# Kernel tuning notes

Hardware: AMD Instinct MI355X
Metric: run time of the kernel (lower is better)

## Reference

```python
import jax, jax.numpy as jnp
import numpy as np
import math

IN_CH = 256
OUT_CH = 256
N_JOINTS = 25
BATCH = 16384


def setup_inputs() -> dict:
    key = jax.random.key(0)
    kx, kw = jax.random.split(key)
    x = jax.random.normal(kx, (N_JOINTS, BATCH, IN_CH), dtype=jnp.float32)
    stdv = 1.0 / math.sqrt(OUT_CH)
    weight = jax.random.uniform(kw, (IN_CH, OUT_CH), dtype=jnp.float32,
                                minval=-stdv, maxval=stdv)
    return {"x": x, "weight": weight}


def reference(x, weight):
    # x: (N, B, D) -> attention over joints N per batch element
    xb = jnp.transpose(x, (1, 0, 2))            # (B, N, D)
    s3 = jnp.einsum('bnd,bmd->bnm', xb, xb)     # (B, N, N) self-similarity
    s = jax.nn.softmax(s3, axis=-1)
    out = jnp.einsum('bnm,bmd->bnd', s, xb)     # (B, N, D)
    out = out @ weight                           # (B, N, out_channels)
    return out
```

## Files before the change

kernel.cpp:

```cpp
#include <hip/hip_runtime.h>

#define GRID   1024
#define BLOCK  256
#define BATCH  16384
#define NJ     25
#define DEPTH  256
#define ITERS  (BATCH / GRID)

typedef short s16x8 __attribute__((ext_vector_type(8)));
typedef short s16x4 __attribute__((ext_vector_type(4)));
typedef float f32x4 __attribute__((ext_vector_type(4)));

__device__ __forceinline__ short f2bf(float f) {
  union { float f; unsigned u; } c; c.f = f;
  unsigned r = (c.u + 0x7FFFu + ((c.u >> 16) & 1u)) >> 16;
  return (short)r;
}

#define MFMA(a, b, c) __builtin_amdgcn_mfma_f32_16x16x32_bf16((a), (b), (c), 0, 0, 0)

__global__ __launch_bounds__(BLOCK, 2)
void geo_gcn_fused(const float* __restrict__ x,
                   const float* __restrict__ w,
                   float* __restrict__ out)
{
  __shared__ short As[32][256];
  __shared__ short Ps[32][40];
  __shared__ float S3[32][36];
  __shared__ short Yt[4][64][32];

  const int tid  = threadIdx.x;
  const int wv   = tid >> 6;
  const int lane = tid & 63;
  const int quad = lane >> 4;
  const int l16  = lane & 15;

  s16x8 wf[8][4];
  {
    const int ncol = wv * 64 + l16;
#pragma unroll
    for (int ks = 0; ks < 8; ++ks)
#pragma unroll
      for (int td = 0; td < 4; ++td) {
        const float* wp = w + (size_t)(ks * 32 + quad * 8) * DEPTH + ncol + td * 16;
#pragma unroll
        for (int j = 0; j < 8; ++j)
          wf[ks][td][j] = f2bf(wp[(size_t)j * DEPTH]);
      }
  }

  const int tm_s = wv >> 1;
  const int tn_s = wv & 1;
  const int srow = tid >> 3;
  const int sq   = tid & 7;
  const int ssw  = (sq ^ (srow & 7)) * 8;

  const float* xb = x + (size_t)srow * BATCH * DEPTH + sq * 8;

  {
    const float* xp = xb + (size_t)blockIdx.x * DEPTH;
#pragma unroll
    for (int c = 0; c < 4; ++c) {
      float4 c0 = make_float4(0.f, 0.f, 0.f, 0.f), c1 = c0;
      if (srow < NJ) {
        c0 = *(const float4*)(xp + c * 64);
        c1 = *(const float4*)(xp + c * 64 + 4);
      }
      s16x8 h;
      h[0]=f2bf(c0.x); h[1]=f2bf(c0.y); h[2]=f2bf(c0.z); h[3]=f2bf(c0.w);
      h[4]=f2bf(c1.x); h[5]=f2bf(c1.y); h[6]=f2bf(c1.z); h[7]=f2bf(c1.w);
      *(s16x8*)&As[srow][ssw + c * 64] = h;
    }
  }
  __syncthreads();

  for (int ib = 0; ib < ITERS; ++ib) {
    const int b = blockIdx.x + GRID * ib;

    float4 nf[8];
#pragma unroll
    for (int i = 0; i < 8; ++i) nf[i] = make_float4(0.f, 0.f, 0.f, 0.f);
    if ((ib + 1 < ITERS) && (srow < NJ)) {
      const float* xp = xb + (size_t)(b + GRID) * DEPTH;
#pragma unroll
      for (int c = 0; c < 4; ++c) {
        nf[2 * c]     = *(const float4*)(xp + c * 64);
        nf[2 * c + 1] = *(const float4*)(xp + c * 64 + 4);
      }
    }

    f32x4 sacc = (f32x4){0.f, 0.f, 0.f, 0.f};
    f32x4 yacc[2][4];
#pragma unroll
    for (int i = 0; i < 2; ++i)
#pragma unroll
      for (int j = 0; j < 4; ++j) yacc[i][j] = (f32x4){0.f, 0.f, 0.f, 0.f};

#pragma unroll
    for (int ks = 0; ks < 8; ++ks) {
      const int co = (((ks * 4 + quad) ^ (l16 & 7)) << 3);
      s16x8 a0 = *(const s16x8*)&As[l16][co];
      s16x8 a1 = *(const s16x8*)&As[16 + l16][co];
      sacc = MFMA(tm_s ? a1 : a0, tn_s ? a1 : a0, sacc);
#pragma unroll
      for (int td = 0; td < 4; ++td) {
        yacc[0][td] = MFMA(a0, wf[ks][td], yacc[0][td]);
        yacc[1][td] = MFMA(a1, wf[ks][td], yacc[1][td]);
      }
    }

#pragma unroll
    for (int r = 0; r < 4; ++r)
      S3[tm_s * 16 + quad * 4 + r][tn_s * 16 + l16] = sacc[r];
    __syncthreads();

    if (ib + 1 < ITERS) {
#pragma unroll
      for (int c = 0; c < 4; ++c) {
        s16x8 h;
        h[0]=f2bf(nf[2*c].x);   h[1]=f2bf(nf[2*c].y);
        h[2]=f2bf(nf[2*c].z);   h[3]=f2bf(nf[2*c].w);
        h[4]=f2bf(nf[2*c+1].x); h[5]=f2bf(nf[2*c+1].y);
        h[6]=f2bf(nf[2*c+1].z); h[7]=f2bf(nf[2*c+1].w);
        *(s16x8*)&As[srow][ssw + c * 64] = h;
      }
    }

    {
      const int row = tid >> 3, c8 = tid & 7;
      float v[4]; float mx = -3.0e38f;
#pragma unroll
      for (int i = 0; i < 4; ++i) {
        const int j = c8 + 8 * i;
        v[i] = (j < NJ) ? S3[row][j] : -3.0e38f;
        mx = fmaxf(mx, v[i]);
      }
      mx = fmaxf(mx, __shfl_xor(mx, 1));
      mx = fmaxf(mx, __shfl_xor(mx, 2));
      mx = fmaxf(mx, __shfl_xor(mx, 4));
      float e[4]; float sum = 0.f;
#pragma unroll
      for (int i = 0; i < 4; ++i) {
        const int j = c8 + 8 * i;
        e[i] = (j < NJ) ? __expf(v[i] - mx) : 0.f;
        sum += e[i];
      }
      sum += __shfl_xor(sum, 1);
      sum += __shfl_xor(sum, 2);
      sum += __shfl_xor(sum, 4);
      const float rinv = 1.0f / sum;
#pragma unroll
      for (int i = 0; i < 4; ++i)
        Ps[row][c8 + 8 * i] = f2bf(e[i] * rinv);
    }
    __syncthreads();

#pragma unroll
    for (int tm = 0; tm < 2; ++tm)
#pragma unroll
      for (int td = 0; td < 4; ++td) {
        s16x4 hy;
#pragma unroll
        for (int r = 0; r < 4; ++r) hy[r] = f2bf(yacc[tm][td][r]);
        const int pc = (tm * 2 + (quad >> 1)) ^ ((l16 >> 1) & 3);
        *(s16x4*)&Yt[wv][td * 16 + l16][pc * 8 + (quad & 1) * 4] = hy;
      }

    s16x8 pf0 = *(const s16x8*)&Ps[l16][quad * 8];
    s16x8 pf1 = *(const s16x8*)&Ps[16 + l16][quad * 8];
    const f32x4 z4 = (f32x4){0.f, 0.f, 0.f, 0.f};
    float* ob = out + (size_t)b * NJ * DEPTH + wv * 64 + l16;
#pragma unroll
    for (int td = 0; td < 4; ++td) {
      const int pr = quad ^ ((l16 >> 1) & 3);
      s16x8 yb = *(const s16x8*)&Yt[wv][td * 16 + l16][pr * 8];
      f32x4 o0 = MFMA(pf0, yb, z4);
      f32x4 o1 = MFMA(pf1, yb, z4);
#pragma unroll
      for (int r = 0; r < 4; ++r) {
        ob[(size_t)(quad * 4 + r) * DEPTH + td * 16] = o0[r];
        const int nr = 16 + quad * 4 + r;
        if (nr < NJ) ob[(size_t)nr * DEPTH + td * 16] = o1[r];
      }
    }
  }
}

extern "C" void kernel_launch(void* const* d_in, const int* in_sizes, int n_in,
                              void* d_out, int out_size, void* d_ws, size_t ws_size,
                              hipStream_t stream) {
  (void)in_sizes; (void)n_in; (void)out_size; (void)d_ws; (void)ws_size;
  const float* x = (const float*)d_in[0];
  const float* w = (const float*)d_in[1];
  float* out = (float*)d_out;
  geo_gcn_fused<<<dim3(GRID), dim3(BLOCK), 0, stream>>>(x, w, out);
}
```

Measured before the change: 712.1 us.

## Stream pre-converted bf16 weight fragments from workspace to raise occupancy

Adds a small pre-pass kernel that converts the fp32 weight into bf16 MFMA fragments laid out in workspace. The main kernel no longer keeps all 32 weight fragments in registers. It reloads two k-slices at a time from global/L2 in a double-buffered, non-unrolled loop, which allows launch bounds of 4 blocks per CU and a grid of 2048. The aim is to raise occupancy and hide memory latency on a bandwidth-bound kernel. The cost is repeated weight loads from cache in every batch iteration plus an extra launch, and the original kernel is kept as a fallback when no workspace is available.

```diff
diff --git a/kernel.cpp b/kernel.cpp
--- a/kernel.cpp
+++ b/kernel.cpp
@@ -1,6 +1,6 @@
 #include <hip/hip_runtime.h>
 
-#define GRID   1024
+#define GRID   2048
 #define BLOCK  256
 #define BATCH  16384
 #define NJ     25
@@ -19,9 +19,24 @@
 
 #define MFMA(a, b, c) __builtin_amdgcn_mfma_f32_16x16x32_bf16((a), (b), (c), 0, 0, 0)
 
-__global__ __launch_bounds__(BLOCK, 2)
+__global__ __launch_bounds__(256)
+void prep_w(const float* __restrict__ w, short* __restrict__ ws) {
+  const int t    = blockIdx.x * 256 + threadIdx.x;
+  const int lane = t & 63;
+  const int td   = (t >> 6) & 3;
+  const int ks   = (t >> 8) & 7;
+  const int wvv  = t >> 11;
+  const int quad = lane >> 4, l16 = lane & 15;
+  const float* wp = w + (size_t)(ks * 32 + quad * 8) * DEPTH + wvv * 64 + td * 16 + l16;
+  s16x8 h;
+#pragma unroll
+  for (int j = 0; j < 8; ++j) h[j] = f2bf(wp[(size_t)j * DEPTH]);
+  *(s16x8*)(ws + (size_t)t * 8) = h;
+}
+
+__global__ __launch_bounds__(BLOCK, 4)
 void geo_gcn_fused(const float* __restrict__ x,
-                   const float* __restrict__ w,
+                   const short* __restrict__ wfrag,
                    float* __restrict__ out)
 {
   __shared__ short As[32][256];
@@ -35,19 +50,7 @@
   const int quad = lane >> 4;
   const int l16  = lane & 15;
 
-  s16x8 wf[8][4];
-  {
-    const int ncol = wv * 64 + l16;
-#pragma unroll
-    for (int ks = 0; ks < 8; ++ks)
-#pragma unroll
-      for (int td = 0; td < 4; ++td) {
-        const float* wp = w + (size_t)(ks * 32 + quad * 8) * DEPTH + ncol + td * 16;
-#pragma unroll
-        for (int j = 0; j < 8; ++j)
-          wf[ks][td][j] = f2bf(wp[(size_t)j * DEPTH]);
-      }
-  }
+  const s16x8* wsv = (const s16x8*)wfrag + (size_t)wv * 2048 + lane;
 
   const int tm_s = wv >> 1;
   const int tn_s = wv & 1;
@@ -96,16 +99,47 @@
 #pragma unroll
       for (int j = 0; j < 4; ++j) yacc[i][j] = (f32x4){0.f, 0.f, 0.f, 0.f};
 
-#pragma unroll
-    for (int ks = 0; ks < 8; ++ks) {
-      const int co = (((ks * 4 + quad) ^ (l16 & 7)) << 3);
-      s16x8 a0 = *(const s16x8*)&As[l16][co];
-      s16x8 a1 = *(const s16x8*)&As[16 + l16][co];
-      sacc = MFMA(tm_s ? a1 : a0, tn_s ? a1 : a0, sacc);
-#pragma unroll
-      for (int td = 0; td < 4; ++td) {
-        yacc[0][td] = MFMA(a0, wf[ks][td], yacc[0][td]);
-        yacc[1][td] = MFMA(a1, wf[ks][td], yacc[1][td]);
+    s16x8 wE[4], wO[4];
+#pragma unroll
+    for (int td = 0; td < 4; ++td) {
+      wE[td] = wsv[td * 64];
+      wO[td] = wsv[256 + td * 64];
+    }
+#pragma unroll 1
+    for (int kp = 0; kp < 4; ++kp) {
+      {
+        const int ks = 2 * kp;
+        const int co = (((ks * 4 + quad) ^ (l16 & 7)) << 3);
+        s16x8 a0 = *(const s16x8*)&As[l16][co];
+        s16x8 a1 = *(const s16x8*)&As[16 + l16][co];
+        sacc = MFMA(tm_s ? a1 : a0, tn_s ? a1 : a0, sacc);
+#pragma unroll
+        for (int td = 0; td < 4; ++td) {
+          yacc[0][td] = MFMA(a0, wE[td], yacc[0][td]);
+          yacc[1][td] = MFMA(a1, wE[td], yacc[1][td]);
+        }
+        if (kp < 3) {
+          const int kn = (ks + 2) * 256;
+#pragma unroll
+          for (int td = 0; td < 4; ++td) wE[td] = wsv[kn + td * 64];
+        }
+      }
+      {
+        const int ks = 2 * kp + 1;
+        const int co = (((ks * 4 + quad) ^ (l16 & 7)) << 3);
+        s16x8 a0 = *(const s16x8*)&As[l16][co];
+        s16x8 a1 = *(const s16x8*)&As[16 + l16][co];
+        sacc = MFMA(tm_s ? a1 : a0, tn_s ? a1 : a0, sacc);
+#pragma unroll
+        for (int td = 0; td < 4; ++td) {
+          yacc[0][td] = MFMA(a0, wO[td], yacc[0][td]);
+          yacc[1][td] = MFMA(a1, wO[td], yacc[1][td]);
+        }
+        if (kp < 3) {
+          const int kn = (ks + 2) * 256;
+#pragma unroll
+          for (int td = 0; td < 4; ++td) wO[td] = wsv[kn + td * 64];
+        }
       }
     }
 
@@ -186,12 +220,176 @@
   }
 }
 
+__global__ __launch_bounds__(BLOCK, 2)
+void geo_gcn_fused_fb(const float* __restrict__ x,
+                      const float* __restrict__ w,
+                      float* __restrict__ out)
+{
+  __shared__ short As[32][256];
+  __shared__ short Ps[32][40];
+  __shared__ float S3[32][36];
+  __shared__ short Yt[4][64][32];
+
+  const int tid  = threadIdx.x;
+  const int wv   = tid >> 6;
+  const int lane = tid & 63;
+  const int quad = lane >> 4;
+  const int l16  = lane & 15;
+
+  s16x8 wf[8][4];
+  {
+    const int ncol = wv * 64 + l16;
+#pragma unroll
+    for (int ks = 0; ks < 8; ++ks)
+#pragma unroll
+      for (int td = 0; td < 4; ++td) {
+        const float* wp = w + (size_t)(ks * 32 + quad * 8) * DEPTH + ncol + td * 16;
+#pragma unroll
+        for (int j = 0; j < 8; ++j)
+          wf[ks][td][j] = f2bf(wp[(size_t)j * DEPTH]);
+      }
+  }
+
+  const int tm_s = wv >> 1;
+  const int tn_s = wv & 1;
+  const int srow = tid >> 3;
+  const int sq   = tid & 7;
+  const int ssw  = (sq ^ (srow & 7)) * 8;
+  const int FITERS = BATCH / GRID;
+
+  const float* xb = x + (size_t)srow * BATCH * DEPTH + sq * 8;
+  {
+    const float* xp = xb + (size_t)blockIdx.x * DEPTH;
+#pragma unroll
+    for (int c = 0; c < 4; ++c) {
+      float4 c0 = make_float4(0.f, 0.f, 0.f, 0.f), c1 = c0;
+      if (srow < NJ) {
+        c0 = *(const float4*)(xp + c * 64);
+        c1 = *(const float4*)(xp + c * 64 + 4);
+      }
+      s16x8 h;
+      h[0]=f2bf(c0.x); h[1]=f2bf(c0.y); h[2]=f2bf(c0.z); h[3]=f2bf(c0.w);
+      h[4]=f2bf(c1.x); h[5]=f2bf(c1.y); h[6]=f2bf(c1.z); h[7]=f2bf(c1.w);
+      *(s16x8*)&As[srow][ssw + c * 64] = h;
+    }
+  }
+  __syncthreads();
+
+  for (int ib = 0; ib < FITERS; ++ib) {
+    const int b = blockIdx.x + GRID * ib;
+    float4 nf[8];
+#pragma unroll
+    for (int i = 0; i < 8; ++i) nf[i] = make_float4(0.f, 0.f, 0.f, 0.f);
+    if ((ib + 1 < FITERS) && (srow < NJ)) {
+      const float* xp = xb + (size_t)(b + GRID) * DEPTH;
+#pragma unroll
+      for (int c = 0; c < 4; ++c) {
+        nf[2 * c]     = *(const float4*)(xp + c * 64);
+        nf[2 * c + 1] = *(const float4*)(xp + c * 64 + 4);
+      }
+    }
+    f32x4 sacc = (f32x4){0.f, 0.f, 0.f, 0.f};
+    f32x4 yacc[2][4];
+#pragma unroll
+    for (int i = 0; i < 2; ++i)
+#pragma unroll
+      for (int j = 0; j < 4; ++j) yacc[i][j] = (f32x4){0.f, 0.f, 0.f, 0.f};
+#pragma unroll
+    for (int ks = 0; ks < 8; ++ks) {
+      const int co = (((ks * 4 + quad) ^ (l16 & 7)) << 3);
+      s16x8 a0 = *(const s16x8*)&As[l16][co];
+      s16x8 a1 = *(const s16x8*)&As[16 + l16][co];
+      sacc = MFMA(tm_s ? a1 : a0, tn_s ? a1 : a0, sacc);
+#pragma unroll
+      for (int td = 0; td < 4; ++td) {
+        yacc[0][td] = MFMA(a0, wf[ks][td], yacc[0][td]);
+        yacc[1][td] = MFMA(a1, wf[ks][td], yacc[1][td]);
+      }
+    }
+#pragma unroll
+    for (int r = 0; r < 4; ++r)
+      S3[tm_s * 16 + quad * 4 + r][tn_s * 16 + l16] = sacc[r];
+    __syncthreads();
+    if (ib + 1 < FITERS) {
+#pragma unroll
+      for (int c = 0; c < 4; ++c) {
+        s16x8 h;
+        h[0]=f2bf(nf[2*c].x);   h[1]=f2bf(nf[2*c].y);
+        h[2]=f2bf(nf[2*c].z);   h[3]=f2bf(nf[2*c].w);
+        h[4]=f2bf(nf[2*c+1].x); h[5]=f2bf(nf[2*c+1].y);
+        h[6]=f2bf(nf[2*c+1].z); h[7]=f2bf(nf[2*c+1].w);
+        *(s16x8*)&As[srow][ssw + c * 64] = h;
+      }
+    }
+    {
+      const int row = tid >> 3, c8 = tid & 7;
+      float v[4]; float mx = -3.0e38f;
+#pragma unroll
+      for (int i = 0; i < 4; ++i) {
+        const int j = c8 + 8 * i;
+        v[i] = (j < NJ) ? S3[row][j] : -3.0e38f;
+        mx = fmaxf(mx, v[i]);
+      }
+      mx = fmaxf(mx, __shfl_xor(mx, 1));
+      mx = fmaxf(mx, __shfl_xor(mx, 2));
+      mx = fmaxf(mx, __shfl_xor(mx, 4));
+      float e[4]; float sum = 0.f;
+#pragma unroll
+      for (int i = 0; i < 4; ++i) {
+        const int j = c8 + 8 * i;
+        e[i] = (j < NJ) ? __expf(v[i] - mx) : 0.f;
+        sum += e[i];
+      }
+      sum += __shfl_xor(sum, 1);
+      sum += __shfl_xor(sum, 2);
+      sum += __shfl_xor(sum, 4);
+      const float rinv = 1.0f / sum;
+#pragma unroll
+      for (int i = 0; i < 4; ++i)
+        Ps[row][c8 + 8 * i] = f2bf(e[i] * rinv);
+    }
+    __syncthreads();
+#pragma unroll
+    for (int tm = 0; tm < 2; ++tm)
+#pragma unroll
+      for (int td = 0; td < 4; ++td) {
+        s16x4 hy;
+#pragma unroll
+        for (int r = 0; r < 4; ++r) hy[r] = f2bf(yacc[tm][td][r]);
+        const int pc = (tm * 2 + (quad >> 1)) ^ ((l16 >> 1) & 3);
+        *(s16x4*)&Yt[wv][td * 16 + l16][pc * 8 + (quad & 1) * 4] = hy;
+      }
+    s16x8 pf0 = *(const s16x8*)&Ps[l16][quad * 8];
+    s16x8 pf1 = *(const s16x8*)&Ps[16 + l16][quad * 8];
+    const f32x4 z4 = (f32x4){0.f, 0.f, 0.f, 0.f};
+    float* ob = out + (size_t)b * NJ * DEPTH + wv * 64 + l16;
+#pragma unroll
+    for (int td = 0; td < 4; ++td) {
+      const int pr = quad ^ ((l16 >> 1) & 3);
+      s16x8 yb = *(const s16x8*)&Yt[wv][td * 16 + l16][pr * 8];
+      f32x4 o0 = MFMA(pf0, yb, z4);
+      f32x4 o1 = MFMA(pf1, yb, z4);
+#pragma unroll
+      for (int r = 0; r < 4; ++r) {
+        ob[(size_t)(quad * 4 + r) * DEPTH + td * 16] = o0[r];
+        const int nr = 16 + quad * 4 + r;
+        if (nr < NJ) ob[(size_t)nr * DEPTH + td * 16] = o1[r];
+      }
+    }
+  }
+}
+
 extern "C" void kernel_launch(void* const* d_in, const int* in_sizes, int n_in,
                               void* d_out, int out_size, void* d_ws, size_t ws_size,
                               hipStream_t stream) {
-  (void)in_sizes; (void)n_in; (void)out_size; (void)d_ws; (void)ws_size;
+  (void)in_sizes; (void)n_in; (void)out_size;
   const float* x = (const float*)d_in[0];
   const float* w = (const float*)d_in[1];
   float* out = (float*)d_out;
-  geo_gcn_fused<<<dim3(GRID), dim3(BLOCK), 0, stream>>>(x, w, out);
-}
+  if (d_ws != nullptr && ws_size >= 131072) {
+    prep_w<<<dim3(32), dim3(256), 0, stream>>>(w, (short*)d_ws);
+    geo_gcn_fused<<<dim3(GRID), dim3(BLOCK), 0, stream>>>(x, (const short*)d_ws, out);
+  } else {
+    geo_gcn_fused_fb<<<dim3(GRID), dim3(BLOCK), 0, stream>>>(x, w, out);
+  }
+}
```

Result: slower. 856.8 us (+20.3%).

## Stage x rows into LDS via direct global-to-LDS DMA, convert to bf16 on read

Applied to the files above, without the earlier changes.

The next batch element's x rows are now copied from global memory straight into an fp32 LDS buffer with global_load_lds, using an XOR-swizzled source layout. This replaces the register prefetch and the pack-to-bf16 step. The bf16 conversion now happens when the MFMA operands are read from LDS, and the Y-tile store to LDS is moved ahead of the softmax barrier. The aim is to save VGPRs and VALU work in the prefetch path. In exchange it doubles the LDS footprint of the A tile, repeats the conversion in every wave, and issues the prefetch later in the iteration, so there is less time to hide its latency.

```diff
diff --git a/kernel.cpp b/kernel.cpp
--- a/kernel.cpp
+++ b/kernel.cpp
@@ -19,12 +19,18 @@
 
 #define MFMA(a, b, c) __builtin_amdgcn_mfma_f32_16x16x32_bf16((a), (b), (c), 0, 0, 0)
 
+__device__ __forceinline__ void dma16(const float* g, float* l) {
+  __builtin_amdgcn_global_load_lds(
+      (const __attribute__((address_space(1))) void*)g,
+      (__attribute__((address_space(3))) void*)l, 16, 0, 0);
+}
+
 __global__ __launch_bounds__(BLOCK, 2)
 void geo_gcn_fused(const float* __restrict__ x,
                    const float* __restrict__ w,
                    float* __restrict__ out)
 {
-  __shared__ short As[32][256];
+  __shared__ float Asf[32][256];
   __shared__ short Ps[32][40];
   __shared__ float S3[32][36];
   __shared__ short Yt[4][64][32];
@@ -51,43 +57,22 @@
 
   const int tm_s = wv >> 1;
   const int tn_s = wv & 1;
-  const int srow = tid >> 3;
-  const int sq   = tid & 7;
-  const int ssw  = (sq ^ (srow & 7)) * 8;
-
-  const float* xb = x + (size_t)srow * BATCH * DEPTH + sq * 8;
 
   {
-    const float* xp = xb + (size_t)blockIdx.x * DEPTH;
+    const float* xe = x + (size_t)blockIdx.x * DEPTH;
 #pragma unroll
-    for (int c = 0; c < 4; ++c) {
-      float4 c0 = make_float4(0.f, 0.f, 0.f, 0.f), c1 = c0;
-      if (srow < NJ) {
-        c0 = *(const float4*)(xp + c * 64);
-        c1 = *(const float4*)(xp + c * 64 + 4);
-      }
-      s16x8 h;
-      h[0]=f2bf(c0.x); h[1]=f2bf(c0.y); h[2]=f2bf(c0.z); h[3]=f2bf(c0.w);
-      h[4]=f2bf(c1.x); h[5]=f2bf(c1.y); h[6]=f2bf(c1.z); h[7]=f2bf(c1.w);
-      *(s16x8*)&As[srow][ssw + c * 64] = h;
+    for (int j = 0; j < 8; ++j) {
+      const int r    = wv * 8 + j;
+      const int nrow = (r < NJ) ? r : (NJ - 1);
+      const float* src = xe + (size_t)nrow * BATCH * DEPTH
+                            + ((lane ^ (2 * (r & 7))) << 2);
+      dma16(src, &Asf[r][0]);
     }
   }
   __syncthreads();
 
   for (int ib = 0; ib < ITERS; ++ib) {
     const int b = blockIdx.x + GRID * ib;
-
-    float4 nf[8];
-#pragma unroll
-    for (int i = 0; i < 8; ++i) nf[i] = make_float4(0.f, 0.f, 0.f, 0.f);
-    if ((ib + 1 < ITERS) && (srow < NJ)) {
-      const float* xp = xb + (size_t)(b + GRID) * DEPTH;
-#pragma unroll
-      for (int c = 0; c < 4; ++c) {
-        nf[2 * c]     = *(const float4*)(xp + c * 64);
-        nf[2 * c + 1] = *(const float4*)(xp + c * 64 + 4);
-      }
-    }
 
     f32x4 sacc = (f32x4){0.f, 0.f, 0.f, 0.f};
     f32x4 yacc[2][4];
@@ -98,9 +83,17 @@
 
 #pragma unroll
     for (int ks = 0; ks < 8; ++ks) {
-      const int co = (((ks * 4 + quad) ^ (l16 & 7)) << 3);
-      s16x8 a0 = *(const s16x8*)&As[l16][co];
-      s16x8 a1 = *(const s16x8*)&As[16 + l16][co];
+      const int g0 = (((4 * ks + quad) ^ (l16 & 7)) << 3);
+      f32x4 ra = *(const f32x4*)&Asf[l16][g0];
+      f32x4 rb = *(const f32x4*)&Asf[l16][g0 + 4];
+      f32x4 rc = *(const f32x4*)&Asf[16 + l16][g0];
+      f32x4 rd = *(const f32x4*)&Asf[16 + l16][g0 + 4];
+      s16x8 a0, a1;
+#pragma unroll
+      for (int j = 0; j < 4; ++j) {
+        a0[j] = f2bf(ra[j]); a0[4 + j] = f2bf(rb[j]);
+        a1[j] = f2bf(rc[j]); a1[4 + j] = f2bf(rd[j]);
+      }
       sacc = MFMA(tm_s ? a1 : a0, tn_s ? a1 : a0, sacc);
 #pragma unroll
       for (int td = 0; td < 4; ++td) {
@@ -115,16 +108,27 @@
     __syncthreads();
 
     if (ib + 1 < ITERS) {
+      const float* xe = x + (size_t)(b + GRID) * DEPTH;
 #pragma unroll
-      for (int c = 0; c < 4; ++c) {
-        s16x8 h;
-        h[0]=f2bf(nf[2*c].x);   h[1]=f2bf(nf[2*c].y);
-        h[2]=f2bf(nf[2*c].z);   h[3]=f2bf(nf[2*c].w);
-        h[4]=f2bf(nf[2*c+1].x); h[5]=f2bf(nf[2*c+1].y);
-        h[6]=f2bf(nf[2*c+1].z); h[7]=f2bf(nf[2*c+1].w);
-        *(s16x8*)&As[srow][ssw + c * 64] = h;
+      for (int j = 0; j < 8; ++j) {
+        const int r    = wv * 8 + j;
+        const int nrow = (r < NJ) ? r : (NJ - 1);
+        const float* src = xe + (size_t)nrow * BATCH * DEPTH
+                              + ((lane ^ (2 * (r & 7))) << 2);
+        dma16(src, &Asf[r][0]);
       }
     }
+
+#pragma unroll
+    for (int tm = 0; tm < 2; ++tm)
+#pragma unroll
+      for (int td = 0; td < 4; ++td) {
+        s16x4 hy;
+#pragma unroll
+        for (int r = 0; r < 4; ++r) hy[r] = f2bf(yacc[tm][td][r]);
+        const int pc = (tm * 2 + (quad >> 1)) ^ ((l16 >> 1) & 3);
+        *(s16x4*)&Yt[wv][td * 16 + l16][pc * 8 + (quad & 1) * 4] = hy;
+      }
 
     {
       const int row = tid >> 3, c8 = tid & 7;
@@ -155,17 +159,6 @@
     }
     __syncthreads();
 
-#pragma unroll
-    for (int tm = 0; tm < 2; ++tm)
-#pragma unroll
-      for (int td = 0; td < 4; ++td) {
-        s16x4 hy;
-#pragma unroll
-        for (int r = 0; r < 4; ++r) hy[r] = f2bf(yacc[tm][td][r]);
-        const int pc = (tm * 2 + (quad >> 1)) ^ ((l16 >> 1) & 3);
-        *(s16x4*)&Yt[wv][td * 16 + l16][pc * 8 + (quad & 1) * 4] = hy;
-      }
-
     s16x8 pf0 = *(const s16x8*)&Ps[l16][quad * 8];
     s16x8 pf1 = *(const s16x8*)&Ps[16 + l16][quad * 8];
     const f32x4 z4 = (f32x4){0.f, 0.f, 0.f, 0.f};
```

Measured after the change: 716.3 us. Within noise of the previous version (+0.6%).
